# Performance work log

Hardware: AMD Instinct MI355X
Metric: run time of the kernel (lower is better)

The kernel has to match this reference:

```python
import jax, jax.numpy as jnp
import numpy as np

B, TA, TV, D, H = 4, 1024, 1024, 512, 8
HD = D // H
SCALE = HD ** -0.5
LN_EPS = 1e-5


def setup_inputs() -> dict:
    key = jax.random.key(0)
    ks = jax.random.split(key, 16)
    init = lambda k, shape, s: (jax.random.normal(k, shape, jnp.float32) * s)
    inp = {
        'q': jax.random.normal(ks[0], (B, TA, D), jnp.float32),
        'k': jax.random.normal(ks[1], (B, TV, D), jnp.float32),
        'v': jax.random.normal(ks[2], (B, TV, D), jnp.float32),
        'guide_map': jax.random.uniform(ks[3], (B, TA, TV), jnp.float32),
        'Wq': init(ks[4], (D, D), D ** -0.5), 'bq': jnp.zeros((D,), jnp.float32),
        'Wk': init(ks[5], (D, D), D ** -0.5), 'bk': jnp.zeros((D,), jnp.float32),
        'Wv': init(ks[6], (D, D), D ** -0.5), 'bv': jnp.zeros((D,), jnp.float32),
        'Wo': init(ks[7], (D, D), D ** -0.5), 'bo': jnp.zeros((D,), jnp.float32),
        'ln_gamma': jnp.ones((D,), jnp.float32),
        'ln_beta': jnp.zeros((D,), jnp.float32),
        'gate': jnp.zeros((1,), jnp.float32),
        'bias_scale': jnp.array(10.0, jnp.float32),
    }
    return inp


def layer_norm(x, gamma, beta):
    mu = jnp.mean(x, axis=-1, keepdims=True)
    var = jnp.mean(jnp.square(x - mu), axis=-1, keepdims=True)
    return (x - mu) * jax.lax.rsqrt(var + LN_EPS) * gamma + beta


def reference(q, k, v, guide_map, Wq, bq, Wk, bk, Wv, bv, Wo, bo, ln_gamma, ln_beta, gate, bias_scale):
    # project and split heads: [B, H, T, hd]
    Q = (q @ Wq.T + bq).reshape(B, TA, H, HD).transpose(0, 2, 1, 3)
    K = (k @ Wk.T + bk).reshape(B, TV, H, HD).transpose(0, 2, 1, 3)
    V = (v @ Wv.T + bv).reshape(B, TV, H, HD).transpose(0, 2, 1, 3)
    scores = jnp.einsum('bhqd,bhkd->bhqk', Q, K) * SCALE
    # transport bias, broadcast over heads (guide_map is [B,Ta,Tv])
    transport_bias = jnp.log(guide_map + 1e-8) * jax.nn.softplus(bias_scale)
    scores = scores + transport_bias[:, None, :, :]
    attn = jax.nn.softmax(scores, axis=-1)  # dropout is identity in eval
    context = jnp.einsum('bhqk,bhkd->bhqd', attn, V)
    context = context.transpose(0, 2, 1, 3).reshape(B, TA, D)
    out = context @ Wo.T + bo
    return layer_norm(q + jax.nn.sigmoid(gate) * out, ln_gamma, ln_beta)
```

## Files before the change

### kernel.cpp

```cpp
#include <hip/hip_runtime.h>
#include <hip/hip_bf16.h>
#include <math.h>

typedef __bf16 bf16_t;
typedef _Float16 hf16_t;
typedef bf16_t bf16x8 __attribute__((ext_vector_type(8)));
typedef bf16_t bf16x4 __attribute__((ext_vector_type(4)));
typedef hf16_t hf16x8 __attribute__((ext_vector_type(8)));
typedef float f32x4 __attribute__((ext_vector_type(4)));
typedef short s16x4 __attribute__((ext_vector_type(4)));

#define B_  4
#define TA_ 1024
#define TV_ 1024
#define D_  512
#define H_  8
#define HD_ 64
#define SCALE_ 0.125f

__device__ inline void g2l16(const void* g, void* l) {
    __builtin_amdgcn_global_load_lds(
        (const __attribute__((address_space(1))) void*)g,
        (__attribute__((address_space(3))) void*)l, 16, 0, 0);
}

__device__ inline f32x4 mfma16_bf16(bf16x4 a, bf16x4 b, f32x4 c) {
    return __builtin_amdgcn_mfma_f32_16x16x16bf16_1k(
        __builtin_bit_cast(s16x4, a), __builtin_bit_cast(s16x4, b), c, 0, 0, 0);
}

__global__ __launch_bounds__(256) void prep_all(
    const float* __restrict__ G, hf16_t* __restrict__ bias_t,
    const float* __restrict__ q, const float* __restrict__ k, const float* __restrict__ v,
    const float* __restrict__ Wq, const float* __restrict__ Wk,
    const float* __restrict__ Wv, const float* __restrict__ Wo,
    bf16_t* __restrict__ qb, bf16_t* __restrict__ kb, bf16_t* __restrict__ vb,
    bf16_t* __restrict__ Wb)
{
    const int tid = threadIdx.x;
    if (blockIdx.x < 1024) {
        __shared__ float Gt[64][68];
        const int kt = blockIdx.x & 15, q64 = (blockIdx.x >> 4) & 15, b = blockIdx.x >> 8;
        const int row = tid >> 4, col4 = (tid & 15) * 4;
        #pragma unroll
        for (int it = 0; it < 4; ++it) {
            int r = it * 16 + row;
            f32x4 g = *(const f32x4*)(G + ((size_t)(b * TA_ + q64 * 64 + r)) * TV_ + kt * 64 + col4);
            *(f32x4*)&Gt[r][col4] = g;
        }
        __syncthreads();
        const int lane = tid & 63, wave = tid >> 6, quad = lane >> 4, l16 = lane & 15;
        hf16x8 lo, hi;
        #pragma unroll
        for (int ct = 0; ct < 4; ++ct) {
            #pragma unroll
            for (int r = 0; r < 4; ++r) {
                float gv = Gt[wave * 16 + l16][ct * 16 + quad * 4 + r];
                float lb = __logf(gv + 1e-8f);
                int idx = ct * 4 + r;
                if (idx < 8) lo[idx] = (hf16_t)lb; else hi[idx - 8] = (hf16_t)lb;
            }
        }
        size_t doff = ((((size_t)b * 16 + kt) * 16 + q64) * 256 + tid) * 16;
        *(hf16x8*)(bias_t + doff) = lo;
        *(hf16x8*)(bias_t + doff + 8) = hi;
    } else {
        const size_t i = ((size_t)(blockIdx.x - 1024) * 256 + tid) * 8;
        const float* src; bf16_t* dst; size_t off;
        const size_t M2 = (size_t)1 << 21;
        if (i < M2)          { src = q; dst = qb; off = i; }
        else if (i < 2 * M2) { src = k; dst = kb; off = i - M2; }
        else if (i < 3 * M2) { src = v; dst = vb; off = i - 2 * M2; }
        else {
            size_t j = i - 3 * M2;
            int wsel = (int)(j >> 18); off = j & 262143;
            src = (wsel == 0) ? Wq : (wsel == 1) ? Wk : (wsel == 2) ? Wv : Wo;
            dst = Wb + ((size_t)wsel << 18);
        }
        f32x4 a = *(const f32x4*)(src + off), c = *(const f32x4*)(src + off + 4);
        bf16x8 r;
        #pragma unroll
        for (int t = 0; t < 4; ++t) { r[t] = (bf16_t)a[t]; r[t + 4] = (bf16_t)c[t]; }
        *(bf16x8*)(dst + off) = r;
    }
}

__device__ inline void gemm128_core(
    const bf16_t* __restrict__ X, const bf16_t* __restrict__ W,
    int mbase, int nbase, bf16_t (*__restrict__ Asm)[128 * 32],
    bf16_t (*__restrict__ Bsm)[128 * 32], f32x4 acc[4][4])
{
    const int tid  = threadIdx.x;
    const int wave = tid >> 6, lane = tid & 63;
    const int quad = lane >> 4, l16 = lane & 15;
    const int wm = wave & 1, wn = wave >> 1;
    const int srow = lane >> 2;
    const int scol = (lane & 3) * 8;

    auto stage = [&](int kt, int buf) {
        const int k0 = kt * 32;
        #pragma unroll
        for (int i = 0; i < 2; ++i) {
            const int row = wave * 32 + i * 16;
            g2l16(X + (size_t)(mbase + row + srow) * D_ + k0 + scol,
                  &Asm[buf][row * 32] + (size_t)lane * 8);
            g2l16(W + (size_t)(nbase + row + srow) * D_ + k0 + scol,
                  &Bsm[buf][row * 32] + (size_t)lane * 8);
        }
    };

    stage(0, 0);
    __syncthreads();
    for (int kt = 0; kt < 16; ++kt) {
        const int buf = kt & 1;
        if (kt < 15) stage(kt + 1, buf ^ 1);
        bf16x8 af[4], bf_[4];
        #pragma unroll
        for (int t = 0; t < 4; ++t) {
            af[t]  = *(const bf16x8*)&Asm[buf][(wm * 64 + t * 16 + l16) * 32 + quad * 8];
            bf_[t] = *(const bf16x8*)&Bsm[buf][(wn * 64 + t * 16 + l16) * 32 + quad * 8];
        }
        #pragma unroll
        for (int mt = 0; mt < 4; ++mt) {
            #pragma unroll
            for (int nt = 0; nt < 4; ++nt)
                acc[mt][nt] = __builtin_amdgcn_mfma_f32_16x16x32_bf16(af[mt], bf_[nt], acc[mt][nt], 0, 0, 0);
        }
        __syncthreads();
    }
}

__global__ __launch_bounds__(256) void gemm_qkv(
    const bf16_t* __restrict__ qb, const bf16_t* __restrict__ kb, const bf16_t* __restrict__ vb,
    const bf16_t* __restrict__ Wb,
    const float* __restrict__ bq, const float* __restrict__ bk, const float* __restrict__ bv,
    bf16_t* __restrict__ Qp, bf16_t* __restrict__ Kp, bf16_t* __restrict__ Vt)
{
    __shared__ bf16_t Asm[2][128 * 32];
    __shared__ bf16_t Bsm[2][128 * 32];

    const int tid  = threadIdx.x;
    const int wave = tid >> 6, lane = tid & 63;
    const int quad = lane >> 4, l16 = lane & 15;
    const int wm = wave & 1, wn = wave >> 1;
    const int mbase = blockIdx.x * 128, nbase = blockIdx.y * 128;
    const int z = blockIdx.z;

    const bf16_t* X   = (z == 0) ? qb : (z == 1) ? kb : vb;
    const float* bias = (z == 0) ? bq : (z == 1) ? bk : bv;
    const bf16_t* W   = Wb + ((size_t)z << 18);

    f32x4 acc[4][4] = {};
    gemm128_core(X, W, mbase, nbase, Asm, Bsm, acc);

    bf16_t* out = (z == 0) ? Qp : (z == 1) ? Kp : Vt;
    #pragma unroll
    for (int mt = 0; mt < 4; ++mt) {
        #pragma unroll
        for (int nt = 0; nt < 4; ++nt) {
            #pragma unroll
            for (int r = 0; r < 4; ++r) {
                int m = mbase + wm * 64 + mt * 16 + quad * 4 + r;
                int n = nbase + wn * 64 + nt * 16 + l16;
                float val = acc[mt][nt][r] + bias[n];
                int b = m >> 10, t = m & 1023, h = n >> 6, hd = n & 63;
                if (z != 2)
                    out[(((size_t)(b * H_ + h) * TA_) + t) * HD_ + hd] = (bf16_t)val;
                else
                    out[((size_t)(b * H_ + h) * HD_ + hd) * TV_ + t] = (bf16_t)val;
            }
        }
    }
}

__global__ __launch_bounds__(512, 4) void attn_kernel(
    const bf16_t* __restrict__ Qp, const bf16_t* __restrict__ Kp,
    const bf16_t* __restrict__ Vt, const hf16_t* __restrict__ bias_t,
    const float* __restrict__ bias_scale, bf16_t* __restrict__ ctx)
{
    __shared__ bf16_t Ksm[2][2][64][72];
    __shared__ bf16_t Vsm[2][2][64][72];

    const int tid  = threadIdx.x;
    const int wave = tid >> 6, lane = tid & 63;
    const int half = wave >> 2, w4 = wave & 3;
    const int quad = lane >> 4, l16 = lane & 15;
    const int bh = blockIdx.x, b = bh >> 3, h = bh & 7;
    const int q64 = blockIdx.y;
    const int t0 = half * 8;
    const int qbase = q64 * 64 + w4 * 16;
    const int rsub = lane >> 3, csub = lane & 7;
    const int shsrc = (lane & 48) | ((lane >> 2) & 12);

    const float sp = log1pf(__expf(bias_scale[0]));

    bf16x8 aq[2];
    #pragma unroll
    for (int s = 0; s < 2; ++s)
        aq[s] = *(const bf16x8*)(Qp + ((size_t)bh * TA_ + qbase + l16) * HD_ + s * 32 + quad * 8);

    f32x4 o[4] = {};
    float m_ = -1e30f, l_ = 0.f;

    auto issue_kv = [&](int kt, bf16x8 kr[2], bf16x8 vr[2]) {
        const int kbase = kt * 64;
        #pragma unroll
        for (int i = 0; i < 2; ++i) {
            int row = w4 * 16 + i * 8 + rsub;
            kr[i] = *(const bf16x8*)(Kp + ((size_t)bh * TV_ + kbase + row) * HD_ + csub * 8);
            vr[i] = *(const bf16x8*)(Vt + ((size_t)bh * HD_ + row) * TV_ + kbase + csub * 8);
        }
    };
    auto write_kv = [&](int buf, bf16x8 kr[2], bf16x8 vr[2]) {
        #pragma unroll
        for (int i = 0; i < 2; ++i) {
            int row = w4 * 16 + i * 8 + rsub;
            *(bf16x8*)&Ksm[half][buf][row][csub * 8] = kr[i];
            *(bf16x8*)&Vsm[half][buf][row][csub * 8] = vr[i];
        }
    };

    const int tidb = (w4 << 6) | lane;
    const hf16_t* bias_base = bias_t + (((size_t)b * 16 * 16 + q64) * 256 + tidb) * 16;
    auto bias_ld = [&](int kt, hf16x8& lo, hf16x8& hi) {
        const hf16_t* bp = bias_base + (size_t)kt * 65536;
        lo = *(const hf16x8*)bp;
        hi = *(const hf16x8*)(bp + 8);
    };
    hf16x8 b0lo, b0hi, b1lo, b1hi;
    bias_ld(t0, b0lo, b0hi);
    bias_ld(t0 + 1, b1lo, b1hi);

    {
        bf16x8 kr[2], vr[2];
        issue_kv(t0, kr, vr);
        write_kv(0, kr, vr);
    }
    __syncthreads();

    auto tile_body = [&](int lk, int buf, hf16x8& slo, hf16x8& shi) {
        const int kt = t0 + lk;
        bf16x8 krn[2], vrn[2];
        if (lk < 7) issue_kv(kt + 1, krn, vrn);
        hf16x8 clo = slo, chi = shi;
        if (lk < 6) bias_ld(kt + 2, slo, shi);

        f32x4 st[4];
        #pragma unroll
        for (int ct = 0; ct < 4; ++ct) {
            f32x4 acc = {};
            #pragma unroll
            for (int s = 0; s < 2; ++s) {
                bf16x8 bk = *(const bf16x8*)&Ksm[half][buf][ct * 16 + l16][s * 32 + quad * 8];
                acc = __builtin_amdgcn_mfma_f32_16x16x32_bf16(bk, aq[s], acc, 0, 0, 0);
            }
            st[ct] = acc;
        }
        float sv[4][4], mx = -1e30f;
        #pragma unroll
        for (int ct = 0; ct < 4; ++ct) {
            #pragma unroll
            for (int r = 0; r < 4; ++r) {
                int idx = ct * 4 + r;
                float lb = (idx < 8) ? (float)clo[idx] : (float)chi[idx - 8];
                float val = fmaf(lb, sp, st[ct][r] * SCALE_);
                sv[ct][r] = val;
                mx = fmaxf(mx, val);
            }
        }
        mx = fmaxf(mx, __shfl_xor(mx, 16, 64));
        mx = fmaxf(mx, __shfl_xor(mx, 32, 64));
        float mn = fmaxf(m_, mx);
        float alpha = __expf(m_ - mn);
        m_ = mn;
        float ls = 0.f;
        #pragma unroll
        for (int ct = 0; ct < 4; ++ct) {
            #pragma unroll
            for (int r = 0; r < 4; ++r) {
                float p = __expf(sv[ct][r] - mn);
                sv[ct][r] = p;
                ls += p;
            }
        }
        ls += __shfl_xor(ls, 16, 64);
        ls += __shfl_xor(ls, 32, 64);
        l_ = l_ * alpha + ls;
        #pragma unroll
        for (int r = 0; r < 4; ++r) {
            float af = __shfl(alpha, shsrc | r, 64);
            #pragma unroll
            for (int dt = 0; dt < 4; ++dt) o[dt][r] *= af;
        }
        #pragma unroll
        for (int ct = 0; ct < 4; ++ct) {
            bf16x4 ap;
            #pragma unroll
            for (int r = 0; r < 4; ++r) ap[r] = (bf16_t)sv[ct][r];
            #pragma unroll
            for (int dt = 0; dt < 4; ++dt) {
                bf16x4 bv = *(const bf16x4*)&Vsm[half][buf][dt * 16 + l16][ct * 16 + quad * 4];
                o[dt] = mfma16_bf16(ap, bv, o[dt]);
            }
        }
        if (lk < 7) write_kv(buf ^ 1, krn, vrn);
        __syncthreads();
    };

    #pragma unroll 1
    for (int kk = 0; kk < 8; kk += 2) {
        tile_body(kk,     0, b0lo, b0hi);
        tile_body(kk + 1, 1, b1lo, b1hi);
    }

    float* cb = (float*)&Ksm[0][0][0][0];
    if (half == 1) {
        float* p = cb + (size_t)tidb * 18;
        #pragma unroll
        for (int dt = 0; dt < 4; ++dt) {
            #pragma unroll
            for (int r = 0; r < 4; ++r) p[dt * 4 + r] = o[dt][r];
        }
        p[16] = m_; p[17] = l_;
    }
    __syncthreads();
    if (half == 0) {
        const float* p = cb + (size_t)tidb * 18;
        float s0[4], s1[4];
        #pragma unroll
        for (int r = 0; r < 4; ++r) {
            float m0 = __shfl(m_, shsrc | r, 64);
            float l0 = __shfl(l_, shsrc | r, 64);
            const float* pr = cb + (size_t)((w4 << 6) | (shsrc | r)) * 18;
            float m1 = pr[16], l1 = pr[17];
            float mm = fmaxf(m0, m1);
            float e0 = __expf(m0 - mm), e1 = __expf(m1 - mm);
            float L = l0 * e0 + l1 * e1;
            s0[r] = e0 / L; s1[r] = e1 / L;
        }
        #pragma unroll
        for (int dt = 0; dt < 4; ++dt) {
            #pragma unroll
            for (int r = 0; r < 4; ++r) {
                float v = o[dt][r] * s0[r] + p[dt * 4 + r] * s1[r];
                int qrow = q64 * 64 + w4 * 16 + quad * 4 + r;
                ctx[((size_t)b * TA_ + qrow) * D_ + h * HD_ + dt * 16 + l16] = (bf16_t)v;
            }
        }
    }
}

__global__ __launch_bounds__(512) void gemm_out_ln(
    const bf16_t* __restrict__ ctx, const bf16_t* __restrict__ Wob,
    const float* __restrict__ bo, const float* __restrict__ q,
    const float* __restrict__ gamma, const float* __restrict__ beta,
    const float* __restrict__ gate, float* __restrict__ y)
{
    __shared__ bf16_t Asm[2][32 * 32];
    __shared__ bf16_t Bsm[2][512 * 32];
    __shared__ float ps[32][4], psq[32][4];

    const int tid  = threadIdx.x;
    const int wave = tid >> 6, lane = tid & 63;
    const int quad = lane >> 4, l16 = lane & 15;
    const int tg = wave & 1, nh = wave >> 1;
    const int mbase = blockIdx.x * 32;

    auto stage = [&](int kt, int buf) {
        const int k0 = kt * 32;
        #pragma unroll
        for (int j = 0; j < 4; ++j) {
            int row0 = wave * 64 + j * 16;
            g2l16(Wob + (size_t)(row0 + (lane >> 2)) * D_ + k0 + (lane & 3) * 8,
                  &Bsm[buf][row0 * 32] + (size_t)lane * 8);
        }
        if (wave < 2) {
            int row0 = wave * 16;
            g2l16(ctx + (size_t)(mbase + row0 + (lane >> 2)) * D_ + k0 + (lane & 3) * 8,
                  &Asm[buf][row0 * 32] + (size_t)lane * 8);
        }
    };

    f32x4 acc[8] = {};
    stage(0, 0);
    __syncthreads();
    for (int kt = 0; kt < 16; ++kt) {
        const int buf = kt & 1;
        if (kt < 15) stage(kt + 1, buf ^ 1);
        bf16x8 af = *(const bf16x8*)&Asm[buf][(tg * 16 + l16) * 32 + quad * 8];
        #pragma unroll
        for (int nt = 0; nt < 8; ++nt) {
            bf16x8 bf_ = *(const bf16x8*)&Bsm[buf][(nh * 128 + nt * 16 + l16) * 32 + quad * 8];
            acc[nt] = __builtin_amdgcn_mfma_f32_16x16x32_bf16(af, bf_, acc[nt], 0, 0, 0);
        }
        __syncthreads();
    }

    const float sg = 1.f / (1.f + __expf(-gate[0]));
    float s[4] = {0.f, 0.f, 0.f, 0.f}, sq[4] = {0.f, 0.f, 0.f, 0.f};
    #pragma unroll
    for (int nt = 0; nt < 8; ++nt) {
        int n = nh * 128 + nt * 16 + l16;
        float bon = bo[n];
        #pragma unroll
        for (int r = 0; r < 4; ++r) {
            int m = mbase + tg * 16 + quad * 4 + r;
            float x = q[(size_t)m * D_ + n] + sg * (acc[nt][r] + bon);
            acc[nt][r] = x;
            s[r] += x; sq[r] += x * x;
        }
    }
    #pragma unroll
    for (int off = 1; off < 16; off <<= 1) {
        #pragma unroll
        for (int r = 0; r < 4; ++r) {
            s[r]  += __shfl_xor(s[r],  off, 64);
            sq[r] += __shfl_xor(sq[r], off, 64);
        }
    }
    if (l16 == 0) {
        #pragma unroll
        for (int r = 0; r < 4; ++r) {
            ps[tg * 16 + quad * 4 + r][nh]  = s[r];
            psq[tg * 16 + quad * 4 + r][nh] = sq[r];
        }
    }
    __syncthreads();
    float mu[4], rstd[4];
    #pragma unroll
    for (int r = 0; r < 4; ++r) {
        int row = tg * 16 + quad * 4 + r;
        float S  = ps[row][0] + ps[row][1] + ps[row][2] + ps[row][3];
        float SQ = psq[row][0] + psq[row][1] + psq[row][2] + psq[row][3];
        mu[r] = S * (1.f / D_);
        float var = SQ * (1.f / D_) - mu[r] * mu[r];
        rstd[r] = rsqrtf(var + 1e-5f);
    }
    #pragma unroll
    for (int nt = 0; nt < 8; ++nt) {
        int n = nh * 128 + nt * 16 + l16;
        float gn = gamma[n], bn = beta[n];
        #pragma unroll
        for (int r = 0; r < 4; ++r) {
            int m = mbase + tg * 16 + quad * 4 + r;
            y[(size_t)m * D_ + n] = (acc[nt][r] - mu[r]) * rstd[r] * gn + bn;
        }
    }
}

extern "C" void kernel_launch(void* const* d_in, const int* in_sizes, int n_in,
                              void* d_out, int out_size, void* d_ws, size_t ws_size,
                              hipStream_t stream) {
    const float* q       = (const float*)d_in[0];
    const float* k       = (const float*)d_in[1];
    const float* v       = (const float*)d_in[2];
    const float* guide   = (const float*)d_in[3];
    const float* Wq      = (const float*)d_in[4];
    const float* bq      = (const float*)d_in[5];
    const float* Wk      = (const float*)d_in[6];
    const float* bk      = (const float*)d_in[7];
    const float* Wv      = (const float*)d_in[8];
    const float* bv      = (const float*)d_in[9];
    const float* Wo      = (const float*)d_in[10];
    const float* bo      = (const float*)d_in[11];
    const float* gamma   = (const float*)d_in[12];
    const float* beta    = (const float*)d_in[13];
    const float* gate    = (const float*)d_in[14];
    const float* bscale  = (const float*)d_in[15];

    char* w = (char*)d_ws;
    bf16_t* qb     = (bf16_t*)(w);
    bf16_t* kb     = (bf16_t*)(w + (4u  << 20));
    bf16_t* vb     = (bf16_t*)(w + (8u  << 20));
    bf16_t* Wb     = (bf16_t*)(w + (12u << 20));
    bf16_t* Qp     = (bf16_t*)(w + (14u << 20));
    bf16_t* Kp     = (bf16_t*)(w + (18u << 20));
    bf16_t* Vt     = (bf16_t*)(w + (22u << 20));
    bf16_t* ctx    = (bf16_t*)(w + (26u << 20));
    hf16_t* bias_t = (hf16_t*)(w + (30u << 20));

    prep_all<<<4608, 256, 0, stream>>>(guide, bias_t, q, k, v, Wq, Wk, Wv, Wo, qb, kb, vb, Wb);
    gemm_qkv<<<dim3(32, 4, 3), 256, 0, stream>>>(qb, kb, vb, Wb, bq, bk, bv, Qp, Kp, Vt);
    attn_kernel<<<dim3(32, 16), 512, 0, stream>>>(Qp, Kp, Vt, bias_t, bscale, ctx);
    gemm_out_ln<<<128, 512, 0, stream>>>(ctx, Wb + ((size_t)3 << 18), bo, q,
                                         gamma, beta, gate, (float*)d_out);
}
```

Baseline: 178.0 us.

## Fuse fp32-to-bf16 conversion into QKV GEMM and merge with prep kernel

Removes the separate bf16 conversion pass over q/k/v and Wq/Wk/Wv. The QKV projection now loads fp32 directly, converts in registers and stores bf16 tiles to LDS, with the next tile's global loads overlapping the MFMA work. The GEMM blocks are merged into the same launch as the guide-map log-bias work and the Wo conversion, so there is one fewer kernel launch. The cost is that the GEMM reads twice as many bytes and gives up async global-to-LDS loads in favour of register staging, which uses more VGPRs.

```diff
diff --git a/kernel.cpp b/kernel.cpp
--- a/kernel.cpp
+++ b/kernel.cpp
@@ -29,17 +29,22 @@
         __builtin_bit_cast(s16x4, a), __builtin_bit_cast(s16x4, b), c, 0, 0, 0);
 }
 
-__global__ __launch_bounds__(256) void prep_all(
+__global__ __launch_bounds__(256) void fused_front(
     const float* __restrict__ G, hf16_t* __restrict__ bias_t,
     const float* __restrict__ q, const float* __restrict__ k, const float* __restrict__ v,
     const float* __restrict__ Wq, const float* __restrict__ Wk,
     const float* __restrict__ Wv, const float* __restrict__ Wo,
-    bf16_t* __restrict__ qb, bf16_t* __restrict__ kb, bf16_t* __restrict__ vb,
-    bf16_t* __restrict__ Wb)
+    const float* __restrict__ bq, const float* __restrict__ bk, const float* __restrict__ bv,
+    bf16_t* __restrict__ Qp, bf16_t* __restrict__ Kp, bf16_t* __restrict__ Vt,
+    bf16_t* __restrict__ Wob)
 {
+    __shared__ bf16_t Asm[2][128 * 32];
+    __shared__ bf16_t Bsm[2][128 * 32];
+
     const int tid = threadIdx.x;
+
     if (blockIdx.x < 1024) {
-        __shared__ float Gt[64][68];
+        float (*Gt)[68] = (float(*)[68])&Asm[0][0];
         const int kt = blockIdx.x & 15, q64 = (blockIdx.x >> 4) & 15, b = blockIdx.x >> 8;
         const int row = tid >> 4, col4 = (tid & 15) * 4;
         #pragma unroll
@@ -64,56 +69,69 @@
         size_t doff = ((((size_t)b * 16 + kt) * 16 + q64) * 256 + tid) * 16;
         *(hf16x8*)(bias_t + doff) = lo;
         *(hf16x8*)(bias_t + doff + 8) = hi;
-    } else {
-        const size_t i = ((size_t)(blockIdx.x - 1024) * 256 + tid) * 8;
-        const float* src; bf16_t* dst; size_t off;
-        const size_t M2 = (size_t)1 << 21;
-        if (i < M2)          { src = q; dst = qb; off = i; }
-        else if (i < 2 * M2) { src = k; dst = kb; off = i - M2; }
-        else if (i < 3 * M2) { src = v; dst = vb; off = i - 2 * M2; }
-        else {
-            size_t j = i - 3 * M2;
-            int wsel = (int)(j >> 18); off = j & 262143;
-            src = (wsel == 0) ? Wq : (wsel == 1) ? Wk : (wsel == 2) ? Wv : Wo;
-            dst = Wb + ((size_t)wsel << 18);
-        }
-        f32x4 a = *(const f32x4*)(src + off), c = *(const f32x4*)(src + off + 4);
+        return;
+    }
+    if (blockIdx.x < 1152) {
+        const size_t j = ((size_t)(blockIdx.x - 1024) * 256 + tid) * 8;
+        f32x4 a = *(const f32x4*)(Wo + j), c = *(const f32x4*)(Wo + j + 4);
         bf16x8 r;
         #pragma unroll
         for (int t = 0; t < 4; ++t) { r[t] = (bf16_t)a[t]; r[t + 4] = (bf16_t)c[t]; }
-        *(bf16x8*)(dst + off) = r;
-    }
-}
-
-__device__ inline void gemm128_core(
-    const bf16_t* __restrict__ X, const bf16_t* __restrict__ W,
-    int mbase, int nbase, bf16_t (*__restrict__ Asm)[128 * 32],
-    bf16_t (*__restrict__ Bsm)[128 * 32], f32x4 acc[4][4])
-{
-    const int tid  = threadIdx.x;
+        *(bf16x8*)(Wob + j) = r;
+        return;
+    }
+
+    const int g = blockIdx.x - 1152;
+    const int z = g >> 7, rem = g & 127;
+    const int mbase = (rem & 31) * 128, nbase = (rem >> 5) * 128;
+    const float* X    = (z == 0) ? q : (z == 1) ? k : v;
+    const float* Wf   = (z == 0) ? Wq : (z == 1) ? Wk : Wv;
+    const float* bias = (z == 0) ? bq : (z == 1) ? bk : bv;
+
     const int wave = tid >> 6, lane = tid & 63;
     const int quad = lane >> 4, l16 = lane & 15;
     const int wm = wave & 1, wn = wave >> 1;
-    const int srow = lane >> 2;
-    const int scol = (lane & 3) * 8;
-
-    auto stage = [&](int kt, int buf) {
+    const int srow = lane >> 2, scol = (lane & 3) * 8;
+
+    f32x4 acc[4][4] = {};
+
+    auto ldt = [&](int kt, f32x4 pa[4], f32x4 pb[4]) {
         const int k0 = kt * 32;
         #pragma unroll
         for (int i = 0; i < 2; ++i) {
-            const int row = wave * 32 + i * 16;
-            g2l16(X + (size_t)(mbase + row + srow) * D_ + k0 + scol,
-                  &Asm[buf][row * 32] + (size_t)lane * 8);
-            g2l16(W + (size_t)(nbase + row + srow) * D_ + k0 + scol,
-                  &Bsm[buf][row * 32] + (size_t)lane * 8);
-        }
-    };
-
-    stage(0, 0);
+            int row = wave * 32 + i * 16 + srow;
+            const float* ap = X + (size_t)(mbase + row) * D_ + k0 + scol;
+            pa[i * 2] = *(const f32x4*)ap; pa[i * 2 + 1] = *(const f32x4*)(ap + 4);
+            const float* bp = Wf + (size_t)(nbase + row) * D_ + k0 + scol;
+            pb[i * 2] = *(const f32x4*)bp; pb[i * 2 + 1] = *(const f32x4*)(bp + 4);
+        }
+    };
+    auto stt = [&](int buf, f32x4 pa[4], f32x4 pb[4]) {
+        #pragma unroll
+        for (int i = 0; i < 2; ++i) {
+            int row = wave * 32 + i * 16 + srow;
+            bf16x8 ra, rb;
+            #pragma unroll
+            for (int t = 0; t < 4; ++t) {
+                ra[t] = (bf16_t)pa[i * 2][t]; ra[t + 4] = (bf16_t)pa[i * 2 + 1][t];
+                rb[t] = (bf16_t)pb[i * 2][t]; rb[t + 4] = (bf16_t)pb[i * 2 + 1][t];
+            }
+            *(bf16x8*)&Asm[buf][row * 32 + scol] = ra;
+            *(bf16x8*)&Bsm[buf][row * 32 + scol] = rb;
+        }
+    };
+
+    {
+        f32x4 pa[4], pb[4];
+        ldt(0, pa, pb);
+        stt(0, pa, pb);
+    }
     __syncthreads();
+    #pragma unroll 1
     for (int kt = 0; kt < 16; ++kt) {
         const int buf = kt & 1;
-        if (kt < 15) stage(kt + 1, buf ^ 1);
+        f32x4 pa[4], pb[4];
+        if (kt < 15) ldt(kt + 1, pa, pb);
         bf16x8 af[4], bf_[4];
         #pragma unroll
         for (int t = 0; t < 4; ++t) {
@@ -126,32 +144,9 @@
             for (int nt = 0; nt < 4; ++nt)
                 acc[mt][nt] = __builtin_amdgcn_mfma_f32_16x16x32_bf16(af[mt], bf_[nt], acc[mt][nt], 0, 0, 0);
         }
+        if (kt < 15) stt(buf ^ 1, pa, pb);
         __syncthreads();
     }
-}
-
-__global__ __launch_bounds__(256) void gemm_qkv(
-    const bf16_t* __restrict__ qb, const bf16_t* __restrict__ kb, const bf16_t* __restrict__ vb,
-    const bf16_t* __restrict__ Wb,
-    const float* __restrict__ bq, const float* __restrict__ bk, const float* __restrict__ bv,
-    bf16_t* __restrict__ Qp, bf16_t* __restrict__ Kp, bf16_t* __restrict__ Vt)
-{
-    __shared__ bf16_t Asm[2][128 * 32];
-    __shared__ bf16_t Bsm[2][128 * 32];
-
-    const int tid  = threadIdx.x;
-    const int wave = tid >> 6, lane = tid & 63;
-    const int quad = lane >> 4, l16 = lane & 15;
-    const int wm = wave & 1, wn = wave >> 1;
-    const int mbase = blockIdx.x * 128, nbase = blockIdx.y * 128;
-    const int z = blockIdx.z;
-
-    const bf16_t* X   = (z == 0) ? qb : (z == 1) ? kb : vb;
-    const float* bias = (z == 0) ? bq : (z == 1) ? bk : bv;
-    const bf16_t* W   = Wb + ((size_t)z << 18);
-
-    f32x4 acc[4][4] = {};
-    gemm128_core(X, W, mbase, nbase, Asm, Bsm, acc);
 
     bf16_t* out = (z == 0) ? Qp : (z == 1) ? Kp : Vt;
     #pragma unroll
@@ -469,19 +464,15 @@
     const float* bscale  = (const float*)d_in[15];
 
     char* w = (char*)d_ws;
-    bf16_t* qb     = (bf16_t*)(w);
-    bf16_t* kb     = (bf16_t*)(w + (4u  << 20));
-    bf16_t* vb     = (bf16_t*)(w + (8u  << 20));
-    bf16_t* Wb     = (bf16_t*)(w + (12u << 20));
-    bf16_t* Qp     = (bf16_t*)(w + (14u << 20));
-    bf16_t* Kp     = (bf16_t*)(w + (18u << 20));
-    bf16_t* Vt     = (bf16_t*)(w + (22u << 20));
-    bf16_t* ctx    = (bf16_t*)(w + (26u << 20));
-    hf16_t* bias_t = (hf16_t*)(w + (30u << 20));
-
-    prep_all<<<4608, 256, 0, stream>>>(guide, bias_t, q, k, v, Wq, Wk, Wv, Wo, qb, kb, vb, Wb);
-    gemm_qkv<<<dim3(32, 4, 3), 256, 0, stream>>>(qb, kb, vb, Wb, bq, bk, bv, Qp, Kp, Vt);
+    bf16_t* Qp     = (bf16_t*)(w);
+    bf16_t* Kp     = (bf16_t*)(w + (4u  << 20));
+    bf16_t* Vt     = (bf16_t*)(w + (8u  << 20));
+    bf16_t* ctx    = (bf16_t*)(w + (12u << 20));
+    hf16_t* bias_t = (hf16_t*)(w + (16u << 20));
+    bf16_t* Wob    = (bf16_t*)(w + (24u << 20));
+
+    fused_front<<<1536, 256, 0, stream>>>(guide, bias_t, q, k, v, Wq, Wk, Wv, Wo,
+                                          bq, bk, bv, Qp, Kp, Vt, Wob);
     attn_kernel<<<dim3(32, 16), 512, 0, stream>>>(Qp, Kp, Vt, bias_t, bscale, ctx);
-    gemm_out_ln<<<128, 512, 0, stream>>>(ctx, Wb + ((size_t)3 << 18), bo, q,
-                                         gamma, beta, gate, (float*)d_out);
-}
+    gemm_out_ln<<<128, 512, 0, stream>>>(ctx, Wob, bo, q, gamma, beta, gate, (float*)d_out);
+}
```

After: 181.6 us. 2.0% more time.
